# Kernel optimization log

Hardware: AMD Instinct MI355X
Metric: run time of the kernel (lower is better)

The kernel has to match this reference:

```python
import jax, jax.numpy as jnp
import numpy as np

T, N, F, H = 32, 1024, 64, 128
GNN_LAYERS = 2  # args.gnn_layers: inner message-passing depth per timestep


def setup_inputs() -> dict:
    key = jax.random.key(0)
    ks = jax.random.split(key, 18)
    w = lambda k, shape: jax.random.normal(k, shape, jnp.float32) * 0.05
    inp = {
        "x": jax.random.normal(ks[0], (1, T, N, F), jnp.float32),
        # dense (soft) adjacency per timestep, scaled ~1/N for stability
        "adjs": jax.random.uniform(ks[1], (1, T, N, N), jnp.float32) / N,
        "edgenum": 16384,
        # input_to_hidden (torch Linear: y = x @ W.T + b)
        "Win_w": w(ks[2], (H, F)), "Win_b": jnp.zeros((H,), jnp.float32),
        # forward GLSTM cell params (gates stacked i|f|o|g along last dim)
        "fWx": w(ks[3], (H, 4 * H)), "fWh": w(ks[4], (H, 4 * H)),
        "fWn": w(ks[5], (H, 4 * H)), "fb": jnp.zeros((4 * H,), jnp.float32),
        # backward GLSTM cell params
        "bWx": w(ks[6], (H, 4 * H)), "bWh": w(ks[7], (H, 4 * H)),
        "bWn": w(ks[8], (H, 4 * H)), "bb": jnp.zeros((4 * H,), jnp.float32),
        # fc0: Linear(2H -> H)
        "fc0_w": w(ks[9], (H, 2 * H)), "fc0_b": jnp.zeros((H,), jnp.float32),
        # w_out: Linear(H -> 1)
        "wout_w": w(ks[10], (1, H)), "wout_b": jnp.zeros((1,), jnp.float32),
    }
    return inp


def _cell(xt, h, c, h_time, adj, Wx, Wh, Wn, b):
    # graph-LSTM cell: neighbor msg = adj @ h_time (per-timestep adjacency)
    z = xt @ Wx + h @ Wh + (adj @ h_time) @ Wn + b  # (N, 4H)
    i, f, o, g = jnp.split(z, 4, axis=-1)
    c2 = jax.nn.sigmoid(f) * c + jax.nn.sigmoid(i) * jnp.tanh(g)
    h2 = jax.nn.sigmoid(o) * jnp.tanh(c2)
    return h2, c2


def _run_direction(xs, adjs, Wx, Wh, Wn, b):
    # xs: (T, N, H); carry = (h_time, c_time); init from first frame of xs
    def step(carry, inputs):
        h_time, c_time = carry
        xt, adj = inputs
        h_l, c_l = h_time, c_time
        for _ in range(GNN_LAYERS):
            h_l, c_l = _cell(xt, h_l, c_l, h_time, adj, Wx, Wh, Wn, b)
        return (h_l, c_l), h_l

    init = (xs[0], xs[0])
    _, hs = jax.lax.scan(step, init, (xs, adjs))
    return hs  # (T, N, H)


def reference(x, adjs, edgenum, Win_w, Win_b, fWx, fWh, fWn, fb,
              bWx, bWh, bWn, bb, fc0_w, fc0_b, wout_w, wout_b):
    batch, seq_len, n, _ = x.shape  # batch == 1
    xs = x[0] @ Win_w.T + Win_b      # (T, N, H)
    a = adjs[0]                       # (T, N, N)

    h_f = _run_direction(xs, a, fWx, fWh, fWn, fb)
    # backward pass: iterate t = T-1 .. 0; outputs stacked in that (reversed)
    # order and concatenated with h_f WITHOUT flipping (faithful to original)
    h_b = _run_direction(xs[::-1], a[::-1], bWx, bWh, bWn, bb)

    out = jnp.concatenate([h_f, h_b], axis=-1) @ fc0_w.T + fc0_b  # (T, N, H)
    y = out[-1] @ wout_w.T + wout_b                               # (N, 1)
    return y.reshape(batch, n, 1)
```

## Files before the change

### kernel.cpp

```cpp
#include <hip/hip_runtime.h>

#define TS 32
#define NN 1024
#define FF 64
#define HH 128
#define H4 512
#define KC 384
#define NBLK 64
#define FRM (HH * NN)
#define ASTR 1032

typedef __attribute__((ext_vector_type(8))) short bf16x8;
typedef __attribute__((ext_vector_type(4))) float f32x4;
typedef __attribute__((ext_vector_type(4))) short s16x4;

static __device__ __forceinline__ float bf2f(short s) {
    union { unsigned int u; float f; } v;
    v.u = ((unsigned int)(unsigned short)s) << 16;
    return v.f;
}
static __device__ __forceinline__ short f2bf(float x) {
    union { float f; unsigned int u; } v; v.f = x;
    unsigned int r = v.u + 0x7fffu + ((v.u >> 16) & 1u);
    return (short)(r >> 16);
}
static __device__ __forceinline__ bf16x8 cvt8(const float* p) {
    f32x4 lo = *(const f32x4*)p;
    f32x4 hi = *(const f32x4*)(p + 4);
    bf16x8 r;
#pragma unroll
    for (int j = 0; j < 4; j++) { r[j] = f2bf(lo[j]); r[4 + j] = f2bf(hi[j]); }
    return r;
}
static __device__ __forceinline__ bf16x8 cvt8v(f32x4 lo, f32x4 hi) {
    bf16x8 r;
#pragma unroll
    for (int j = 0; j < 4; j++) { r[j] = f2bf(lo[j]); r[4 + j] = f2bf(hi[j]); }
    return r;
}
static __device__ __forceinline__ f32x4 ldnt4(const float* p) {
    return __builtin_nontemporal_load((const f32x4*)p);
}
static __device__ __forceinline__ float frcp(float x) {
    float r; asm("v_rcp_f32 %0, %1" : "=v"(r) : "v"(x)); return r;
}
static __device__ __forceinline__ float sigm(float x) { return frcp(1.0f + __expf(-x)); }
static __device__ __forceinline__ float tanhfast(float x) { return 1.0f - 2.0f * frcp(__expf(2.0f * x) + 1.0f); }
static __device__ __forceinline__ f32x4 MFMA(bf16x8 a, bf16x8 b, f32x4 c) {
    return __builtin_amdgcn_mfma_f32_16x16x32_bf16(a, b, c, 0, 0, 0);
}

__global__ __launch_bounds__(256) void k_pre(
    const float* __restrict__ x, const float* __restrict__ winw,
    const float* __restrict__ winb,
    const float* __restrict__ fWx, const float* __restrict__ fWn,
    const float* __restrict__ fWh,
    const float* __restrict__ bWx, const float* __restrict__ bWn,
    const float* __restrict__ bWh,
    const float* __restrict__ fc0_w, const float* __restrict__ fc0_b,
    const float* __restrict__ wout_w, const float* __restrict__ wout_b,
    short* __restrict__ xs, short* __restrict__ hTf0, short* __restrict__ hTb0,
    short* __restrict__ WcatT_f, short* __restrict__ WcatT_b,
    float* __restrict__ vsh_g, unsigned int* __restrict__ flags,
    float* __restrict__ out) {
    const int b = blockIdx.x;
    const int tid = threadIdx.x;
    if (b < 512) {
        const int wv = tid >> 6, lane = tid & 63;
        const int quad = lane >> 4, l16 = lane & 15;
        const int row0 = b * 64 + wv * 16;
        f32x4 acc[8];
#pragma unroll
        for (int i = 0; i < 8; i++) acc[i] = (f32x4){0.f, 0.f, 0.f, 0.f};
#pragma unroll
        for (int kt = 0; kt < 2; kt++) {
            const int k = kt * 32 + quad * 8;
            bf16x8 a = cvt8(x + (size_t)(row0 + l16) * FF + k);
#pragma unroll
            for (int nt = 0; nt < 8; nt++) {
                bf16x8 bb = cvt8(winw + (size_t)(nt * 16 + l16) * FF + k);
                acc[nt] = MFMA(a, bb, acc[nt]);
            }
        }
#pragma unroll
        for (int nt = 0; nt < 8; nt++) {
            const int hcol = nt * 16 + l16;
            const float bias = winb[hcol];
#pragma unroll
            for (int r = 0; r < 4; r++) {
                const int row = row0 + quad * 4 + r;
                const short v = f2bf(acc[nt][r] + bias);
                xs[(size_t)row * HH + hcol] = v;
                const int frame = row >> 10, nrow = row & 1023;
                if (frame == 0) hTf0[(size_t)hcol * NN + nrow] = v;
                else if (frame == TS - 1) hTb0[(size_t)hcol * NN + nrow] = v;
            }
        }
    } else if (b < 608) {
        __shared__ __align__(16) short tile[64][72];
        const int b2 = b - 512;
        const int half = b2 / 48, sub = b2 % 48;
        const float* Wx = half ? bWx : fWx;
        const float* Wn = half ? bWn : fWn;
        const float* Wh = half ? bWh : fWh;
        short* dst = half ? WcatT_b : WcatT_f;
        const int n0 = (sub / 6) * 64, k0 = (sub % 6) * 64;
        for (int i = tid; i < 512; i += 256) {
            const int r = i >> 3, cc = i & 7;
            const int kg = k0 + r;
            const float* m = (kg < 128) ? Wx : (kg < 256 ? Wn : Wh);
            *(bf16x8*)&tile[r][cc * 8] = cvt8(m + (size_t)(kg & 127) * H4 + n0 + cc * 8);
        }
        __syncthreads();
        for (int i = tid; i < 512; i += 256) {
            const int rr = i >> 3, kk = i & 7;
            bf16x8 o;
#pragma unroll
            for (int j = 0; j < 8; j++) o[j] = tile[kk * 8 + j][rr];
            *(bf16x8*)(dst + (size_t)(n0 + rr) * KC + k0 + kk * 8) = o;
        }
    } else {
        float a = 0.f;
        for (int i = 0; i < HH; i++) a += wout_w[i] * fc0_w[(size_t)i * 256 + tid];
        vsh_g[tid] = a;
        if (tid == 0) {
            float s = wout_b[0];
            for (int i = 0; i < HH; i++) s += wout_w[i] * fc0_b[i];
            vsh_g[256] = s;
        }
        for (int i = tid; i < 128; i += 256) flags[i] = 0u;
        for (int i = tid; i < NN; i += 256) out[i] = 0.f;
    }
}

__global__ __launch_bounds__(512)
__attribute__((amdgpu_waves_per_eu(2, 2))) void k_main(
    const float* __restrict__ adjs, const short* __restrict__ xs,
    const short* __restrict__ WcT_f, const short* __restrict__ WcT_b,
    const float* __restrict__ bias_f, const float* __restrict__ bias_b,
    short* __restrict__ hTf, short* __restrict__ hTb,
    const float* __restrict__ vsh_g, unsigned int* __restrict__ flags,
    float* __restrict__ out) {
    __shared__ __align__(16) short wg[12 * 4 * HH * 8];
    __shared__ __align__(16) short adjT[16 * ASTR];
    __shared__ __align__(16) short Acat[16][392];

    const int tid = threadIdx.x;
    const int wv = tid >> 6, lane = tid & 63, quad = lane >> 4, l16 = lane & 15;
    const int dir = blockIdx.x >> 6, bslot = blockIdx.x & 63, R = bslot * 16;
    const short* WcT  = dir ? WcT_b : WcT_f;
    const float* bias = dir ? bias_b : bias_f;
    short* hTd = dir ? hTb : hTf;
    unsigned int* myflags = flags + dir * 64;
    const int hcol = wv * 16 + l16;

    bf16x8 wr0[12], wr1[12], wr2[12];
#pragma unroll
    for (int kt = 0; kt < 12; kt++) {
        wr0[kt] = *(const bf16x8*)(WcT + (size_t)(0 * HH + hcol) * KC + kt * 32 + quad * 8);
        wr1[kt] = *(const bf16x8*)(WcT + (size_t)(1 * HH + hcol) * KC + kt * 32 + quad * 8);
        wr2[kt] = *(const bf16x8*)(WcT + (size_t)(2 * HH + hcol) * KC + kt * 32 + quad * 8);
    }
    for (int i = tid; i < 6144; i += 512) {
        const int kt = i >> 9, rem = i & 511, qd = rem >> 7, hc = rem & 127;
        *(bf16x8*)&wg[(size_t)i * 8] =
            *(const bf16x8*)(WcT + (size_t)(3 * HH + hc) * KC + kt * 32 + qd * 8);
    }
    const float bi  = bias[hcol];
    const float bf_ = bias[HH + hcol];
    const float bo  = bias[2 * HH + hcol];
    const float bg_ = bias[3 * HH + hcol];

    const int frame0 = dir ? (TS - 1) : 0;
    if (tid < 256) {
        const int r = tid >> 4, cc = tid & 15;
        *(bf16x8*)&Acat[r][256 + cc * 8] =
            *(const bf16x8*)(xs + ((size_t)frame0 * NN + R + r) * HH + cc * 8);
    }
    const int ar = tid & 15, ac = tid >> 4;
    {
        const float* asrc = adjs + (size_t)frame0 * NN * NN + (size_t)(R + ar) * NN + ac * 32;
        f32x4 p0[8];
#pragma unroll
        for (int j = 0; j < 8; j++) p0[j] = ldnt4(asrc + j * 4);
#pragma unroll
        for (int j = 0; j < 4; j++)
            *(bf16x8*)&adjT[ar * ASTR + ac * 32 + j * 8] = cvt8v(p0[2 * j], p0[2 * j + 1]);
    }
    __syncthreads();
    float creg[4];
#pragma unroll
    for (int r = 0; r < 4; r++) creg[r] = bf2f(Acat[quad * 4 + r][256 + hcol]);

    f32x4 pf[8];
    for (int t = 0; t < TS; t++) {
        const int frame = dir ? (TS - 1 - t) : t;
        const short* xs_t = xs + (size_t)frame * NN * HH;
        const short* hTi = hTd + (size_t)t * FRM;
        short* hTo       = hTd + (size_t)(t + 1) * FRM;

        if (tid < 256) {
            const int r = tid >> 4, cc = tid & 15;
            *(bf16x8*)&Acat[r][cc * 8] =
                *(const bf16x8*)(xs_t + (size_t)(R + r) * HH + cc * 8);
        }
        if (t < TS - 1) {
            const int nf = dir ? (TS - 2 - t) : (t + 1);
            const float* asrc = adjs + (size_t)nf * NN * NN + (size_t)(R + ar) * NN + ac * 32;
#pragma unroll
            for (int j = 0; j < 8; j++) pf[j] = ldnt4(asrc + j * 4);
        }

        f32x4 an0 = (f32x4){0.f, 0.f, 0.f, 0.f};
        f32x4 an1 = (f32x4){0.f, 0.f, 0.f, 0.f};
        {
            const short* hbase = hTi + (size_t)hcol * NN;
            const unsigned long long FULL = 0x1111111111111111ull;
            unsigned long long done = 0ull;
            do {
                unsigned int v = __hip_atomic_load(myflags + lane, __ATOMIC_RELAXED,
                                                   __HIP_MEMORY_SCOPE_AGENT);
                unsigned long long arrived = __ballot(v >= (unsigned int)t);
                unsigned long long grp = arrived & (arrived >> 1) & (arrived >> 2)
                                       & (arrived >> 3) & FULL;
                unsigned long long todo = grp & ~done;
                done |= todo;
                asm volatile("" ::: "memory");
                while (todo) {
                    const int b = (int)__ffsll((unsigned long long)todo) - 1;
                    todo &= todo - 1;
                    const int kt = b >> 1;
                    bf16x8 a0 = *(const bf16x8*)&adjT[l16 * ASTR + kt * 32 + quad * 8];
                    bf16x8 b0 = *(const bf16x8*)(hbase + kt * 32 + quad * 8);
                    an0 = MFMA(a0, b0, an0);
                    bf16x8 a1 = *(const bf16x8*)&adjT[l16 * ASTR + (kt + 1) * 32 + quad * 8];
                    bf16x8 b1 = *(const bf16x8*)(hbase + (kt + 1) * 32 + quad * 8);
                    an1 = MFMA(a1, b1, an1);
                }
            } while (done != FULL);
        }
#pragma unroll
        for (int r = 0; r < 4; r++) Acat[quad * 4 + r][HH + hcol] = f2bf(an0[r] + an1[r]);
        __syncthreads();

        if (t < TS - 1) {
#pragma unroll
            for (int j = 0; j < 4; j++)
                *(bf16x8*)&adjT[ar * ASTR + ac * 32 + j * 8] = cvt8v(pf[2 * j], pf[2 * j + 1]);
        }

#pragma unroll
        for (int l = 0; l < 2; l++) {
            f32x4 az0 = (f32x4){0.f, 0.f, 0.f, 0.f};
            f32x4 az1 = az0, az2 = az0, az3 = az0;
#pragma unroll
            for (int kt = 0; kt < 12; kt++) {
                bf16x8 a = *(const bf16x8*)&Acat[l16][kt * 32 + quad * 8];
                az0 = MFMA(a, wr0[kt], az0);
                az1 = MFMA(a, wr1[kt], az1);
                az2 = MFMA(a, wr2[kt], az2);
                bf16x8 b3 = *(const bf16x8*)&wg[((size_t)kt * 512 + quad * 128 + hcol) * 8];
                az3 = MFMA(a, b3, az3);
            }
            short hbf[4];
#pragma unroll
            for (int r = 0; r < 4; r++) {
                const float cn = sigm(az1[r] + bf_) * creg[r]
                               + sigm(az0[r] + bi) * tanhfast(az3[r] + bg_);
                creg[r] = cn;
                hbf[r] = f2bf(sigm(az2[r] + bo) * tanhfast(cn));
            }
            if (l == 1) {
                union { s16x4 v; unsigned long long u; } pk;
#pragma unroll
                for (int r = 0; r < 4; r++) pk.v[r] = hbf[r];
                __hip_atomic_store(
                    (unsigned long long*)(hTo + (size_t)hcol * NN + R + quad * 4),
                    pk.u, __ATOMIC_RELAXED, __HIP_MEMORY_SCOPE_AGENT);
            }
            __syncthreads();
#pragma unroll
            for (int r = 0; r < 4; r++) Acat[quad * 4 + r][256 + hcol] = hbf[r];
            if (l == 0) __syncthreads();
        }
        asm volatile("s_waitcnt vmcnt(0)" ::: "memory");
        __syncthreads();
        if (tid == 0)
            __hip_atomic_store(myflags + bslot, (unsigned int)(t + 1),
                               __ATOMIC_RELEASE, __HIP_MEMORY_SCOPE_AGENT);
    }

    if (tid < 256) {
        const int r = tid >> 4, j = tid & 15;
        float p = 0.f;
        for (int k = j * 8; k < j * 8 + 8; k++)
            p += bf2f(Acat[r][256 + k]) * vsh_g[dir * HH + k];
#pragma unroll
        for (int off = 8; off; off >>= 1) p += __shfl_down(p, off, 16);
        if (j == 0) atomicAdd(&out[R + r], p + (dir ? 0.f : vsh_g[256]));
    }
}

extern "C" void kernel_launch(void* const* d_in, const int* in_sizes, int n_in,
                              void* d_out, int out_size, void* d_ws, size_t ws_size,
                              hipStream_t stream) {
    const float* x      = (const float*)d_in[0];
    const float* adjs   = (const float*)d_in[1];
    const float* win_w  = (const float*)d_in[3];
    const float* win_b  = (const float*)d_in[4];
    const float* fWx    = (const float*)d_in[5];
    const float* fWh    = (const float*)d_in[6];
    const float* fWn    = (const float*)d_in[7];
    const float* fb     = (const float*)d_in[8];
    const float* bWx    = (const float*)d_in[9];
    const float* bWh    = (const float*)d_in[10];
    const float* bWn    = (const float*)d_in[11];
    const float* bb     = (const float*)d_in[12];
    const float* fc0_w  = (const float*)d_in[13];
    const float* fc0_b  = (const float*)d_in[14];
    const float* wout_w = (const float*)d_in[15];
    const float* wout_b = (const float*)d_in[16];

    char* ws = (char*)d_ws;
    size_t off = 0;
    auto alloc = [&](size_t bytes) -> void* {
        void* p = ws + off;
        off += (bytes + 255) & ~(size_t)255;
        return p;
    };
    short* xs      = (short*)alloc((size_t)TS * NN * HH * 2);
    short* WcatT_f = (short*)alloc((size_t)H4 * KC * 2);
    short* WcatT_b = (short*)alloc((size_t)H4 * KC * 2);
    short* hTf     = (short*)alloc((size_t)(TS + 1) * FRM * 2);
    short* hTb     = (short*)alloc((size_t)(TS + 1) * FRM * 2);
    float* vsh_g   = (float*)alloc(257 * 4);
    unsigned int* flags = (unsigned int*)alloc(512);
    float* outp    = (float*)d_out;

    hipLaunchKernelGGL(k_pre, dim3(609), dim3(256), 0, stream,
                       x, win_w, win_b, fWx, fWn, fWh, bWx, bWn, bWh,
                       fc0_w, fc0_b, wout_w, wout_b,
                       xs, hTf, hTb, WcatT_f, WcatT_b, vsh_g, flags, outp);

    void* args[] = {
        (void*)&adjs, (void*)&xs, (void*)&WcatT_f, (void*)&WcatT_b,
        (void*)&fb, (void*)&bb,
        (void*)&hTf, (void*)&hTb,
        (void*)&vsh_g, (void*)&flags, (void*)&outp,
    };
    hipLaunchCooperativeKernel((void*)k_main, dim3(128), dim3(512), args, 0, stream);
}
```

Baseline: 897.6 us.

## Precompute x and h partial gate products before neighbor wait, reuse x part across layers

The x-projection (k-tiles 0-3) and the recurrent-h projection (k-tiles 8-11) of the gate matmul are now computed before spin-waiting on other blocks' hidden states, so that work overlaps the inter-block synchronization. The x contribution is computed once and shared by both GNN layers instead of being recomputed. Weight fragments for three gates are no longer held in registers; they are read from global/L2 each time, which frees VGPRs but adds memory traffic. The adjacency prefetch is moved after the neighbor aggregation, and an extra barrier is added.

Result: slower. 1.124 ms (+25.3%).

```diff
diff --git a/kernel.cpp b/kernel.cpp
--- a/kernel.cpp
+++ b/kernel.cpp
@@ -154,13 +154,11 @@
     unsigned int* myflags = flags + dir * 64;
     const int hcol = wv * 16 + l16;
 
-    bf16x8 wr0[12], wr1[12], wr2[12];
-#pragma unroll
-    for (int kt = 0; kt < 12; kt++) {
-        wr0[kt] = *(const bf16x8*)(WcT + (size_t)(0 * HH + hcol) * KC + kt * 32 + quad * 8);
-        wr1[kt] = *(const bf16x8*)(WcT + (size_t)(1 * HH + hcol) * KC + kt * 32 + quad * 8);
-        wr2[kt] = *(const bf16x8*)(WcT + (size_t)(2 * HH + hcol) * KC + kt * 32 + quad * 8);
-    }
+    const short* wp0 = WcT + (size_t)hcol * KC + quad * 8;
+    const short* wp1 = wp0 + (size_t)HH * KC;
+    const short* wp2 = wp1 + (size_t)HH * KC;
+    const int wgb = (quad * 128 + hcol) * 8;
+
     for (int i = tid; i < 6144; i += 512) {
         const int kt = i >> 9, rem = i & 511, qd = rem >> 7, hc = rem & 127;
         *(bf16x8*)&wg[(size_t)i * 8] =
@@ -204,11 +202,26 @@
             *(bf16x8*)&Acat[r][cc * 8] =
                 *(const bf16x8*)(xs_t + (size_t)(R + r) * HH + cc * 8);
         }
-        if (t < TS - 1) {
-            const int nf = dir ? (TS - 2 - t) : (t + 1);
-            const float* asrc = adjs + (size_t)nf * NN * NN + (size_t)(R + ar) * NN + ac * 32;
-#pragma unroll
-            for (int j = 0; j < 8; j++) pf[j] = ldnt4(asrc + j * 4);
+        __syncthreads();
+
+        f32x4 xa0 = (f32x4){0.f, 0.f, 0.f, 0.f};
+        f32x4 xa1 = xa0, xa2 = xa0, xa3 = xa0;
+#pragma unroll
+        for (int kt = 0; kt < 4; kt++) {
+            bf16x8 a = *(const bf16x8*)&Acat[l16][kt * 32 + quad * 8];
+            xa0 = MFMA(a, *(const bf16x8*)(wp0 + kt * 32), xa0);
+            xa1 = MFMA(a, *(const bf16x8*)(wp1 + kt * 32), xa1);
+            xa2 = MFMA(a, *(const bf16x8*)(wp2 + kt * 32), xa2);
+            xa3 = MFMA(a, *(const bf16x8*)&wg[kt * 4096 + wgb], xa3);
+        }
+        f32x4 l00 = xa0, l01 = xa1, l02 = xa2, l03 = xa3;
+#pragma unroll
+        for (int kt = 8; kt < 12; kt++) {
+            bf16x8 a = *(const bf16x8*)&Acat[l16][kt * 32 + quad * 8];
+            l00 = MFMA(a, *(const bf16x8*)(wp0 + kt * 32), l00);
+            l01 = MFMA(a, *(const bf16x8*)(wp1 + kt * 32), l01);
+            l02 = MFMA(a, *(const bf16x8*)(wp2 + kt * 32), l02);
+            l03 = MFMA(a, *(const bf16x8*)&wg[kt * 4096 + wgb], l03);
         }
 
         f32x4 an0 = (f32x4){0.f, 0.f, 0.f, 0.f};
@@ -244,45 +257,65 @@
         __syncthreads();
 
         if (t < TS - 1) {
+            const int nf = dir ? (TS - 2 - t) : (t + 1);
+            const float* asrc = adjs + (size_t)nf * NN * NN + (size_t)(R + ar) * NN + ac * 32;
+#pragma unroll
+            for (int j = 0; j < 8; j++) pf[j] = ldnt4(asrc + j * 4);
+        }
+
+#pragma unroll
+        for (int kt = 4; kt < 8; kt++) {
+            bf16x8 a = *(const bf16x8*)&Acat[l16][kt * 32 + quad * 8];
+            l00 = MFMA(a, *(const bf16x8*)(wp0 + kt * 32), l00);
+            l01 = MFMA(a, *(const bf16x8*)(wp1 + kt * 32), l01);
+            l02 = MFMA(a, *(const bf16x8*)(wp2 + kt * 32), l02);
+            l03 = MFMA(a, *(const bf16x8*)&wg[kt * 4096 + wgb], l03);
+        }
+        short hbf[4];
+#pragma unroll
+        for (int r = 0; r < 4; r++) {
+            const float cn = sigm(l01[r] + bf_) * creg[r]
+                           + sigm(l00[r] + bi) * tanhfast(l03[r] + bg_);
+            creg[r] = cn;
+            hbf[r] = f2bf(sigm(l02[r] + bo) * tanhfast(cn));
+        }
+#pragma unroll
+        for (int r = 0; r < 4; r++) Acat[quad * 4 + r][256 + hcol] = hbf[r];
+        __syncthreads();
+
+        f32x4 l10 = xa0, l11 = xa1, l12 = xa2, l13 = xa3;
+#pragma unroll
+        for (int kt = 4; kt < 12; kt++) {
+            bf16x8 a = *(const bf16x8*)&Acat[l16][kt * 32 + quad * 8];
+            l10 = MFMA(a, *(const bf16x8*)(wp0 + kt * 32), l10);
+            l11 = MFMA(a, *(const bf16x8*)(wp1 + kt * 32), l11);
+            l12 = MFMA(a, *(const bf16x8*)(wp2 + kt * 32), l12);
+            l13 = MFMA(a, *(const bf16x8*)&wg[kt * 4096 + wgb], l13);
+        }
+#pragma unroll
+        for (int r = 0; r < 4; r++) {
+            const float cn = sigm(l11[r] + bf_) * creg[r]
+                           + sigm(l10[r] + bi) * tanhfast(l13[r] + bg_);
+            creg[r] = cn;
+            hbf[r] = f2bf(sigm(l12[r] + bo) * tanhfast(cn));
+        }
+        {
+            union { s16x4 v; unsigned long long u; } pk;
+#pragma unroll
+            for (int r = 0; r < 4; r++) pk.v[r] = hbf[r];
+            __hip_atomic_store(
+                (unsigned long long*)(hTo + (size_t)hcol * NN + R + quad * 4),
+                pk.u, __ATOMIC_RELAXED, __HIP_MEMORY_SCOPE_AGENT);
+        }
+        if (t < TS - 1) {
 #pragma unroll
             for (int j = 0; j < 4; j++)
                 *(bf16x8*)&adjT[ar * ASTR + ac * 32 + j * 8] = cvt8v(pf[2 * j], pf[2 * j + 1]);
         }
-
-#pragma unroll
-        for (int l = 0; l < 2; l++) {
-            f32x4 az0 = (f32x4){0.f, 0.f, 0.f, 0.f};
-            f32x4 az1 = az0, az2 = az0, az3 = az0;
-#pragma unroll
-            for (int kt = 0; kt < 12; kt++) {
-                bf16x8 a = *(const bf16x8*)&Acat[l16][kt * 32 + quad * 8];
-                az0 = MFMA(a, wr0[kt], az0);
-                az1 = MFMA(a, wr1[kt], az1);
-                az2 = MFMA(a, wr2[kt], az2);
-                bf16x8 b3 = *(const bf16x8*)&wg[((size_t)kt * 512 + quad * 128 + hcol) * 8];
-                az3 = MFMA(a, b3, az3);
-            }
-            short hbf[4];
-#pragma unroll
-            for (int r = 0; r < 4; r++) {
-                const float cn = sigm(az1[r] + bf_) * creg[r]
-                               + sigm(az0[r] + bi) * tanhfast(az3[r] + bg_);
-                creg[r] = cn;
-                hbf[r] = f2bf(sigm(az2[r] + bo) * tanhfast(cn));
-            }
-            if (l == 1) {
-                union { s16x4 v; unsigned long long u; } pk;
-#pragma unroll
-                for (int r = 0; r < 4; r++) pk.v[r] = hbf[r];
-                __hip_atomic_store(
-                    (unsigned long long*)(hTo + (size_t)hcol * NN + R + quad * 4),
-                    pk.u, __ATOMIC_RELAXED, __HIP_MEMORY_SCOPE_AGENT);
-            }
-            __syncthreads();
-#pragma unroll
-            for (int r = 0; r < 4; r++) Acat[quad * 4 + r][256 + hcol] = hbf[r];
-            if (l == 0) __syncthreads();
-        }
+        __syncthreads();
+#pragma unroll
+        for (int r = 0; r < 4; r++) Acat[quad * 4 + r][256 + hcol] = hbf[r];
+
         asm volatile("s_waitcnt vmcnt(0)" ::: "memory");
         __syncthreads();
         if (tid == 0)
```
